# Kernel optimization log

Measured on AMD Instinct MI355X. Metric: run time of the kernel, lower is better.

Reference implementation:

```python
import jax, jax.numpy as jnp
import numpy as np

N = 10000      # nodes
E = 640000     # edges (avg degree 64)
D = 128        # embedding_size
L = 3          # num_layers=4 -> 1 + (4-2) = 3 conv layers


def setup_inputs() -> dict:
    key = jax.random.key(0)
    ks = jax.random.split(key, 4)
    z = jax.random.normal(ks[0], (N, D), dtype=jnp.float32)
    edge_index = jax.random.randint(ks[1], (2, E), 0, N, dtype=jnp.int32)
    # per-layer GCN weights/bias and LayerNorm affine params, stacked over layers
    Ws = jax.random.normal(ks[2], (L, D, D), dtype=jnp.float32) / np.sqrt(D).astype(np.float32)
    bs = jnp.zeros((L, D), dtype=jnp.float32)
    gammas = jnp.ones((L, D), dtype=jnp.float32)
    betas = jnp.zeros((L, D), dtype=jnp.float32)
    return {"z": z, "edge_index": edge_index, "Ws": Ws, "bs": bs,
            "gammas": gammas, "betas": betas}


def _layernorm(x, g, b, eps=1e-5):
    mu = jnp.mean(x, axis=-1, keepdims=True)
    var = jnp.var(x, axis=-1, keepdims=True)
    return (x - mu) * jax.lax.rsqrt(var + eps) * g + b


def reference(z, edge_index, Ws, bs, gammas, betas):
    # GCNConv (PyG default): add self-loops, symmetric normalization
    loops = jnp.arange(N, dtype=edge_index.dtype)
    src = jnp.concatenate([edge_index[0], loops])   # [E+N]
    dst = jnp.concatenate([edge_index[1], loops])   # [E+N]
    deg = jax.ops.segment_sum(jnp.ones(src.shape[0], z.dtype), dst, num_segments=N)
    dinv = jax.lax.rsqrt(jnp.maximum(deg, 1.0))
    norm = dinv[src] * dinv[dst]                    # [E+N]

    x = z
    for i in range(L):
        xw = x @ Ws[i]                              # [N, D] dense transform
        msg = xw[src] * norm[:, None]               # gather + scale  [E+N, D]
        x = jax.ops.segment_sum(msg, dst, num_segments=N) + bs[i]  # scatter-add
        x = _layernorm(x, gammas[i], betas[i])
        x = jax.nn.gelu(x)
        # F.dropout(p=0.1) omitted: deterministic eval-mode reference
    return x
```

## Files before the change

kernel.cpp:

```cpp
#include <hip/hip_runtime.h>

#define DD 128
#define D2 64
#define BW_DST 32
#define BW_SHIFT 5
#define BATCH 4096
#define NBPAD 320
#define P2CAP 6144

struct alignas(8) Rec { unsigned int meta; float w; };

__device__ __forceinline__ unsigned int bf16rne(float f) {
    unsigned int u = __float_as_uint(f);
    unsigned int r = ((u >> 16) & 1u) + 0x7fffu;
    return (u + r) >> 16;
}
__device__ __forceinline__ float bflo(unsigned int v) { return __uint_as_float(v << 16); }
__device__ __forceinline__ float bfhi(unsigned int v) { return __uint_as_float(v & 0xFFFF0000u); }


__global__ __launch_bounds__(256) void bucket_count(
    const int* __restrict__ dst, int E, int* __restrict__ bsum, int NB)
{
    __shared__ int cnt[NBPAD];
    int t = threadIdx.x;
    for (int b = t; b < NB; b += 256) cnt[b] = 0;
    __syncthreads();
    int gtid = blockIdx.x * 256 + t, gsz = gridDim.x * 256;
    for (int e = gtid; e < E; e += gsz) atomicAdd(&cnt[dst[e] >> BW_SHIFT], 1);
    __syncthreads();
    for (int b = t; b < NB; b += 256) if (cnt[b]) atomicAdd(&bsum[b], cnt[b]);
}

__global__ void scan_bsum(const int* __restrict__ bsum, int* __restrict__ bbase,
                          int* __restrict__ bcur, int* __restrict__ row_ptr,
                          int NB, int N, int E)
{
    __shared__ int part[256];
    int t = threadIdx.x;
    int chunk = (NB + 255) / 256;
    int lo = t * chunk, hi = min(lo + chunk, NB);
    int s = 0;
    for (int b = lo; b < hi; ++b) s += bsum[b];
    part[t] = s;
    __syncthreads();
    for (int o = 1; o < 256; o <<= 1) {
        int v = (t >= o) ? part[t - o] : 0;
        __syncthreads();
        part[t] += v;
        __syncthreads();
    }
    int run = (t == 0) ? 0 : part[t - 1];
    for (int b = lo; b < hi; ++b) {
        bbase[b] = run;
        bcur[b] = run;
        run += bsum[b];
    }
    if (t == 0) row_ptr[N] = E;
}

__global__ __launch_bounds__(256) void bucket_fill(
    const int* __restrict__ src, const int* __restrict__ dst, int E,
    int* __restrict__ bcur, unsigned int* __restrict__ bcsr, int NB)
{
    __shared__ unsigned short sbkt[BATCH];
    __shared__ unsigned short sbkt2[BATCH];
    __shared__ int cnt[NBPAD];
    __shared__ int boff[NBPAD];
    __shared__ int gbase[NBPAD];
    __shared__ int lcur[NBPAD];
    __shared__ unsigned int staged[BATCH];
    int t = threadIdx.x;

    for (int base = blockIdx.x * BATCH; base < E; base += gridDim.x * BATCH) {
        int n = min(E - base, BATCH);
        for (int b = t; b < NBPAD; b += 256) cnt[b] = 0;
        __syncthreads();
        for (int i = t; i < n; i += 256) {
            int d = dst[base + i];
            int bk = d >> BW_SHIFT;
            sbkt[i] = (unsigned short)bk;
            atomicAdd(&cnt[bk], 1);
        }
        __syncthreads();
        if (t < 64) {
            int lo = t * 5;
            int c0 = cnt[lo], c1 = cnt[lo + 1], c2 = cnt[lo + 2],
                c3 = cnt[lo + 3], c4 = cnt[lo + 4];
            int s = c0 + c1 + c2 + c3 + c4;
            int v = s;
            #pragma unroll
            for (int o = 1; o < 64; o <<= 1) { int u = __shfl_up(v, o, 64); if (t >= o) v += u; }
            int e0 = v - s;
            int e1 = e0 + c0, e2 = e1 + c1, e3 = e2 + c2, e4 = e3 + c3;
            boff[lo] = e0; boff[lo + 1] = e1; boff[lo + 2] = e2;
            boff[lo + 3] = e3; boff[lo + 4] = e4;
            lcur[lo] = e0; lcur[lo + 1] = e1; lcur[lo + 2] = e2;
            lcur[lo + 3] = e3; lcur[lo + 4] = e4;
            if (c0) gbase[lo]     = atomicAdd(&bcur[lo],     c0);
            if (c1) gbase[lo + 1] = atomicAdd(&bcur[lo + 1], c1);
            if (c2) gbase[lo + 2] = atomicAdd(&bcur[lo + 2], c2);
            if (c3) gbase[lo + 3] = atomicAdd(&bcur[lo + 3], c3);
            if (c4) gbase[lo + 4] = atomicAdd(&bcur[lo + 4], c4);
        }
        __syncthreads();
        for (int i = t; i < n; i += 256) {
            int e = base + i;
            int ss = src[e], dd = dst[e];
            int bk = sbkt[i];
            int p = atomicAdd(&lcur[bk], 1);
            staged[p] = (unsigned int)ss | ((unsigned int)(dd & (BW_DST - 1)) << 27);
            sbkt2[p] = (unsigned short)bk;
        }
        __syncthreads();
        for (int i = t; i < n; i += 256) {
            int bk = sbkt2[i];
            bcsr[gbase[bk] + (i - boff[bk])] = staged[i];
        }
        __syncthreads();
    }
}

__global__ __launch_bounds__(256) void fine_sort(
    const int* __restrict__ bbase, const unsigned int* __restrict__ bcsr,
    unsigned int* __restrict__ csr4, int* __restrict__ row_ptr,
    float* __restrict__ dinv, int N, int NB, int E)
{
    __shared__ unsigned int staged[P2CAP];
    __shared__ int dcnt[BW_DST];
    __shared__ int dcur[BW_DST];
    int b = blockIdx.x;
    int d0 = b << BW_SHIFT;
    int nd = min(BW_DST, N - d0);
    int base = bbase[b];
    int end  = (b + 1 < NB) ? bbase[b + 1] : E;
    int cnt  = end - base;
    int t = threadIdx.x;
    if (t < BW_DST) dcnt[t] = 0;
    __syncthreads();
    for (int i = t; i < cnt; i += 256) atomicAdd(&dcnt[bcsr[base + i] >> 27], 1);
    __syncthreads();
    if (t < BW_DST) {
        int c = dcnt[t];
        int v = c;
        #pragma unroll
        for (int o = 1; o < BW_DST; o <<= 1) { int u = __shfl_up(v, o, BW_DST); if (t >= o) v += u; }
        int loff = v - c;
        if (t < nd) {
            int node = d0 + t;
            row_ptr[node] = base + loff;
            dinv[node] = rsqrtf((float)(c + 1));
        }
        dcur[t] = loff;
    }
    __syncthreads();
    if (cnt <= P2CAP) {
        for (int i = t; i < cnt; i += 256) {
            unsigned int r = bcsr[base + i];
            int p = atomicAdd(&dcur[r >> 27], 1);
            staged[p] = r;
        }
        __syncthreads();
        for (int i = t; i < cnt; i += 256) csr4[base + i] = staged[i];
    } else {
        for (int i = t; i < cnt; i += 256) {
            unsigned int r = bcsr[base + i];
            int p = atomicAdd(&dcur[r >> 27], 1);
            csr4[base + p] = r;
        }
    }
}

__global__ __launch_bounds__(256) void weight_fill(
    const int* __restrict__ bbase, const unsigned int* __restrict__ csr4,
    const float* __restrict__ dinv, Rec* __restrict__ csr, int NB, int N, int E)
{
    int b = blockIdx.x;
    int base = bbase[b];
    int end  = (b + 1 < NB) ? bbase[b + 1] : E;
    int d0 = b << BW_SHIFT;
    for (int i = base + threadIdx.x; i < end; i += 256) {
        unsigned int r = csr4[i];
        int s = r & 0x07FFFFFFu;
        int d = d0 + (int)(r >> 27);
        Rec rec;
        rec.meta = r;
        rec.w = dinv[s] * dinv[d];
        csr[i] = rec;
    }
}


#define GR 16
__global__ void gemm_xw(const float* __restrict__ x, const float* __restrict__ W,
                        unsigned int* __restrict__ xwb, int N) {
    __shared__ float xs[GR][DD];
    int t = threadIdx.x;
    int r0 = blockIdx.x * GR;
    #pragma unroll
    for (int r = 0; r < GR; ++r) {
        int row = r0 + r;
        xs[r][t] = (row < N) ? x[row * DD + t] : 0.f;
    }
    __syncthreads();
    float acc[GR];
    #pragma unroll
    for (int r = 0; r < GR; ++r) acc[r] = 0.f;
    for (int k = 0; k < DD; k += 4) {
        float w0 = W[(k + 0) * DD + t];
        float w1 = W[(k + 1) * DD + t];
        float w2 = W[(k + 2) * DD + t];
        float w3 = W[(k + 3) * DD + t];
        #pragma unroll
        for (int r = 0; r < GR; ++r) {
            float4 xv = *(const float4*)&xs[r][k];
            acc[r] = fmaf(xv.x, w0, acc[r]);
            acc[r] = fmaf(xv.y, w1, acc[r]);
            acc[r] = fmaf(xv.z, w2, acc[r]);
            acc[r] = fmaf(xv.w, w3, acc[r]);
        }
    }
    #pragma unroll
    for (int r = 0; r < GR; ++r) {
        int row = r0 + r;
        float other = __shfl_xor(acc[r], 1);
        if (row < N && !(t & 1)) {
            unsigned int p = bf16rne(acc[r]) | (bf16rne(other) << 16);
            xwb[row * D2 + (t >> 1)] = p;
        }
    }
}

__global__ __launch_bounds__(512) void agg_gemm(
    const unsigned int* __restrict__ xwb_in, const Rec* __restrict__ csr,
    const int* __restrict__ row_ptr, const float* __restrict__ dinv,
    const float* __restrict__ bias, const float* __restrict__ gamma,
    const float* __restrict__ beta, const float* __restrict__ W,
    unsigned int* __restrict__ xwb_out, int N)
{
    __shared__ float xs[8][DD];
    int t = threadIdx.x;
    int wid = t >> 6, l = t & 63;
    int i = blockIdx.x * 8 + wid;
    if (i < N) {
        int beg = row_ptr[i], end = row_ptr[i + 1];
        float ax = 0.f, ay = 0.f;
        #pragma unroll 8
        for (int j = beg; j < end; ++j) {
            Rec er = csr[j];
            unsigned int v = xwb_in[(er.meta & 0x07FFFFFFu) * D2 + l];
            ax = fmaf(bflo(v), er.w, ax);
            ay = fmaf(bfhi(v), er.w, ay);
        }
        float di = dinv[i], sn = di * di;
        unsigned int v = xwb_in[i * D2 + l];
        ax = fmaf(bflo(v), sn, ax);
        ay = fmaf(bfhi(v), sn, ay);
        float2 b2 = ((const float2*)bias)[l];
        ax += b2.x; ay += b2.y;
        float sum = ax + ay, sq = ax * ax + ay * ay;
        #pragma unroll
        for (int o = 32; o > 0; o >>= 1) { sum += __shfl_xor(sum, o); sq += __shfl_xor(sq, o); }
        float mu   = sum * (1.f / DD);
        float var  = sq * (1.f / DD) - mu * mu;
        float rstd = rsqrtf(var + 1e-5f);
        float2 g2  = ((const float2*)gamma)[l];
        float2 be2 = ((const float2*)beta)[l];
        float y0 = (ax - mu) * rstd * g2.x + be2.x;
        float y1 = (ay - mu) * rstd * g2.y + be2.y;
        y0 = 0.5f * y0 * (1.f + tanhf(0.7978845608f * (y0 + 0.044715f * y0 * y0 * y0)));
        y1 = 0.5f * y1 * (1.f + tanhf(0.7978845608f * (y1 + 0.044715f * y1 * y1 * y1)));
        xs[wid][2 * l]     = y0;
        xs[wid][2 * l + 1] = y1;
    } else {
        xs[wid][2 * l]     = 0.f;
        xs[wid][2 * l + 1] = 0.f;
    }
    __syncthreads();
    int col = t & 127, h = t >> 7;
    float a0 = 0.f, a1 = 0.f;
    for (int k = 0; k < DD; k += 4) {
        float w0 = W[(k + 0) * DD + col];
        float w1 = W[(k + 1) * DD + col];
        float w2 = W[(k + 2) * DD + col];
        float w3 = W[(k + 3) * DD + col];
        float4 x0 = *(const float4*)&xs[h * 2 + 0][k];
        float4 x1 = *(const float4*)&xs[h * 2 + 1][k];
        a0 = fmaf(x0.x, w0, a0); a0 = fmaf(x0.y, w1, a0);
        a0 = fmaf(x0.z, w2, a0); a0 = fmaf(x0.w, w3, a0);
        a1 = fmaf(x1.x, w0, a1); a1 = fmaf(x1.y, w1, a1);
        a1 = fmaf(x1.z, w2, a1); a1 = fmaf(x1.w, w3, a1);
    }
    int row0 = blockIdx.x * 8 + h * 2;
    float o0 = __shfl_xor(a0, 1);
    float o1 = __shfl_xor(a1, 1);
    if (!(t & 1)) {
        if (row0 < N)
            xwb_out[row0 * D2 + (col >> 1)] = bf16rne(a0) | (bf16rne(o0) << 16);
        if (row0 + 1 < N)
            xwb_out[(row0 + 1) * D2 + (col >> 1)] = bf16rne(a1) | (bf16rne(o1) << 16);
    }
}

__global__ __launch_bounds__(256) void agg_ln_gelu(
    const unsigned int* __restrict__ xwb, const Rec* __restrict__ csr,
    const int* __restrict__ row_ptr, const float* __restrict__ dinv,
    const float* __restrict__ bias, const float* __restrict__ gamma,
    const float* __restrict__ beta, float* __restrict__ out, int N)
{
    int i = blockIdx.x * 4 + (threadIdx.x >> 6);
    if (i >= N) return;
    int l = threadIdx.x & 63;
    int beg = row_ptr[i], end = row_ptr[i + 1];
    float ax = 0.f, ay = 0.f;
    #pragma unroll 8
    for (int j = beg; j < end; ++j) {
        Rec er = csr[j];
        unsigned int v = xwb[(er.meta & 0x07FFFFFFu) * D2 + l];
        ax = fmaf(bflo(v), er.w, ax);
        ay = fmaf(bfhi(v), er.w, ay);
    }
    float di = dinv[i], sn = di * di;
    unsigned int v = xwb[i * D2 + l];
    ax = fmaf(bflo(v), sn, ax);
    ay = fmaf(bfhi(v), sn, ay);
    float2 b2 = ((const float2*)bias)[l];
    ax += b2.x; ay += b2.y;
    float sum = ax + ay, sq = ax * ax + ay * ay;
    #pragma unroll
    for (int o = 32; o > 0; o >>= 1) { sum += __shfl_xor(sum, o); sq += __shfl_xor(sq, o); }
    float mu   = sum * (1.f / DD);
    float var  = sq * (1.f / DD) - mu * mu;
    float rstd = rsqrtf(var + 1e-5f);
    float2 g2  = ((const float2*)gamma)[l];
    float2 be2 = ((const float2*)beta)[l];
    float y0 = (ax - mu) * rstd * g2.x + be2.x;
    float y1 = (ay - mu) * rstd * g2.y + be2.y;
    y0 = 0.5f * y0 * (1.f + tanhf(0.7978845608f * (y0 + 0.044715f * y0 * y0 * y0)));
    y1 = 0.5f * y1 * (1.f + tanhf(0.7978845608f * (y1 + 0.044715f * y1 * y1 * y1)));
    float2 o2; o2.x = y0; o2.y = y1;
    ((float2*)out)[i * D2 + l] = o2;
}

static inline size_t align_up(size_t x, size_t a) { return (x + a - 1) & ~(a - 1); }

extern "C" void kernel_launch(void* const* d_in, const int* in_sizes, int n_in,
                              void* d_out, int out_size, void* d_ws, size_t ws_size,
                              hipStream_t stream) {
    const float* z      = (const float*)d_in[0];
    const int*   ei     = (const int*)d_in[1];
    const float* Ws     = (const float*)d_in[2];
    const float* bs     = (const float*)d_in[3];
    const float* gammas = (const float*)d_in[4];
    const float* betas  = (const float*)d_in[5];

    int E  = in_sizes[1] / 2;
    int LD = in_sizes[3];
    int Dd = in_sizes[2] / LD;
    int L  = LD / Dd;
    int N  = in_sizes[0] / Dd;
    int NB = (N + BW_DST - 1) / BW_DST;

    const int* srcp = ei;
    const int* dstp = ei + E;

    char* ws = (char*)d_ws;
    size_t off = 0;
    int* bsum = (int*)(ws + off);        off = align_up(off + (size_t)NBPAD * 4, 256);
    int* bbase = (int*)(ws + off);       off = align_up(off + (size_t)NBPAD * 4, 256);
    int* bcur = (int*)(ws + off);        off = align_up(off + (size_t)NBPAD * 4, 256);
    float* dinv = (float*)(ws + off);    off = align_up(off + (size_t)N * 4, 256);
    int* row_ptr = (int*)(ws + off);     off = align_up(off + (size_t)(N + 1) * 4, 256);
    unsigned int* bcsr = (unsigned int*)(ws + off); off = align_up(off + (size_t)E * 4, 256);
    unsigned int* csr4 = (unsigned int*)(ws + off); off = align_up(off + (size_t)E * 4, 256);
    Rec* csr = (Rec*)(ws + off);         off = align_up(off + (size_t)E * 8, 256);
    unsigned int* xwb_a = (unsigned int*)(ws + off); off = align_up(off + (size_t)N * D2 * 4, 256);
    unsigned int* xwb_b = (unsigned int*)(ws + off); off = align_up(off + (size_t)N * D2 * 4, 256);
    float* dout = (float*)d_out;
    (void)ws_size; (void)n_in; (void)out_size;

    int nb_p1 = (E + BATCH - 1) / BATCH;

    hipMemsetAsync(bsum, 0, (size_t)NBPAD * 4, stream);
    bucket_count<<<160, 256, 0, stream>>>(dstp, E, bsum, NB);
    scan_bsum<<<1, 256, 0, stream>>>(bsum, bbase, bcur, row_ptr, NB, N, E);
    bucket_fill<<<nb_p1, 256, 0, stream>>>(srcp, dstp, E, bcur, bcsr, NB);
    fine_sort<<<NB, 256, 0, stream>>>(bbase, bcsr, csr4, row_ptr, dinv, N, NB, E);
    weight_fill<<<NB, 256, 0, stream>>>(bbase, csr4, dinv, csr, NB, N, E);

    gemm_xw<<<(N + GR - 1) / GR, DD, 0, stream>>>(z, Ws, xwb_a, N);

    unsigned int* tin = xwb_a;
    unsigned int* tout = xwb_b;
    for (int li = 0; li < L - 1; ++li) {
        agg_gemm<<<(N + 7) / 8, 512, 0, stream>>>(
            tin, csr, row_ptr, dinv,
            bs + (size_t)li * Dd, gammas + (size_t)li * Dd, betas + (size_t)li * Dd,
            Ws + (size_t)(li + 1) * Dd * Dd, tout, N);
        unsigned int* tmp = tin; tin = tout; tout = tmp;
    }

    agg_ln_gelu<<<(N + 3) / 4, 256, 0, stream>>>(tin, csr, row_ptr, dinv,
                                                 bs + (size_t)(L - 1) * Dd,
                                                 gammas + (size_t)(L - 1) * Dd,
                                                 betas + (size_t)(L - 1) * Dd, dout, N);
}
```

Measured before the change: 166.8 us.

## Replace count pass with fixed-capacity buckets and scan after fill

Removes the separate bucket-count pass and its memset. Each coarse bucket now gets a fixed-capacity slot region (CAP entries) in the staging buffer, and the exclusive scan runs after the fill, using the final bucket cursors. Fine sort reads from the fixed slot region and writes to the compacted offsets. The batch size is also halved. This saves a full read of the dst array and one launch, but it relies on no bucket exceeding CAP entries (about 2048 are expected at this input size) and uses a larger staging buffer.

Result: no change. 169.5 us (+1.6%).

```diff
diff --git a/kernel.cpp b/kernel.cpp
--- a/kernel.cpp
+++ b/kernel.cpp
@@ -4,8 +4,9 @@
 #define D2 64
 #define BW_DST 32
 #define BW_SHIFT 5
-#define BATCH 4096
+#define BATCH 2048
 #define NBPAD 320
+#define CAP 4096
 #define P2CAP 6144
 
 struct alignas(8) Rec { unsigned int meta; float w; };
@@ -18,45 +19,8 @@
 __device__ __forceinline__ float bflo(unsigned int v) { return __uint_as_float(v << 16); }
 __device__ __forceinline__ float bfhi(unsigned int v) { return __uint_as_float(v & 0xFFFF0000u); }
 
-
-__global__ __launch_bounds__(256) void bucket_count(
-    const int* __restrict__ dst, int E, int* __restrict__ bsum, int NB)
-{
-    __shared__ int cnt[NBPAD];
-    int t = threadIdx.x;
-    for (int b = t; b < NB; b += 256) cnt[b] = 0;
-    __syncthreads();
-    int gtid = blockIdx.x * 256 + t, gsz = gridDim.x * 256;
-    for (int e = gtid; e < E; e += gsz) atomicAdd(&cnt[dst[e] >> BW_SHIFT], 1);
-    __syncthreads();
-    for (int b = t; b < NB; b += 256) if (cnt[b]) atomicAdd(&bsum[b], cnt[b]);
-}
-
-__global__ void scan_bsum(const int* __restrict__ bsum, int* __restrict__ bbase,
-                          int* __restrict__ bcur, int* __restrict__ row_ptr,
-                          int NB, int N, int E)
-{
-    __shared__ int part[256];
-    int t = threadIdx.x;
-    int chunk = (NB + 255) / 256;
-    int lo = t * chunk, hi = min(lo + chunk, NB);
-    int s = 0;
-    for (int b = lo; b < hi; ++b) s += bsum[b];
-    part[t] = s;
-    __syncthreads();
-    for (int o = 1; o < 256; o <<= 1) {
-        int v = (t >= o) ? part[t - o] : 0;
-        __syncthreads();
-        part[t] += v;
-        __syncthreads();
-    }
-    int run = (t == 0) ? 0 : part[t - 1];
-    for (int b = lo; b < hi; ++b) {
-        bbase[b] = run;
-        bcur[b] = run;
-        run += bsum[b];
-    }
-    if (t == 0) row_ptr[N] = E;
+__global__ void init_bcur(int* __restrict__ bcur) {
+    bcur[threadIdx.x] = (int)threadIdx.x * CAP;
 }
 
 __global__ __launch_bounds__(256) void bucket_fill(
@@ -121,8 +85,34 @@
     }
 }
 
+__global__ void scan_cnt(const int* __restrict__ bcur, int* __restrict__ bbase,
+                         int* __restrict__ row_ptr, int NB, int N, int E)
+{
+    __shared__ int part[256];
+    int t = threadIdx.x;
+    int chunk = (NB + 255) / 256;
+    int lo = t * chunk, hi = min(lo + chunk, NB);
+    int s = 0;
+    for (int b = lo; b < hi; ++b) s += bcur[b] - b * CAP;
+    part[t] = s;
+    __syncthreads();
+    for (int o = 1; o < 256; o <<= 1) {
+        int v = (t >= o) ? part[t - o] : 0;
+        __syncthreads();
+        part[t] += v;
+        __syncthreads();
+    }
+    int run = (t == 0) ? 0 : part[t - 1];
+    for (int b = lo; b < hi; ++b) {
+        bbase[b] = run;
+        run += bcur[b] - b * CAP;
+    }
+    if (t == 0) row_ptr[N] = E;
+}
+
 __global__ __launch_bounds__(256) void fine_sort(
-    const int* __restrict__ bbase, const unsigned int* __restrict__ bcsr,
+    const int* __restrict__ bcur, const int* __restrict__ bbase,
+    const unsigned int* __restrict__ bcsr,
     unsigned int* __restrict__ csr4, int* __restrict__ row_ptr,
     float* __restrict__ dinv, int N, int NB, int E)
 {
@@ -132,13 +122,13 @@
     int b = blockIdx.x;
     int d0 = b << BW_SHIFT;
     int nd = min(BW_DST, N - d0);
-    int base = bbase[b];
-    int end  = (b + 1 < NB) ? bbase[b + 1] : E;
-    int cnt  = end - base;
+    int base_in = b * CAP;
+    int cnt = bcur[b] - base_in;
+    int gout = bbase[b];
     int t = threadIdx.x;
     if (t < BW_DST) dcnt[t] = 0;
     __syncthreads();
-    for (int i = t; i < cnt; i += 256) atomicAdd(&dcnt[bcsr[base + i] >> 27], 1);
+    for (int i = t; i < cnt; i += 256) atomicAdd(&dcnt[bcsr[base_in + i] >> 27], 1);
     __syncthreads();
     if (t < BW_DST) {
         int c = dcnt[t];
@@ -148,7 +138,7 @@
         int loff = v - c;
         if (t < nd) {
             int node = d0 + t;
-            row_ptr[node] = base + loff;
+            row_ptr[node] = gout + loff;
             dinv[node] = rsqrtf((float)(c + 1));
         }
         dcur[t] = loff;
@@ -156,17 +146,17 @@
     __syncthreads();
     if (cnt <= P2CAP) {
         for (int i = t; i < cnt; i += 256) {
-            unsigned int r = bcsr[base + i];
+            unsigned int r = bcsr[base_in + i];
             int p = atomicAdd(&dcur[r >> 27], 1);
             staged[p] = r;
         }
         __syncthreads();
-        for (int i = t; i < cnt; i += 256) csr4[base + i] = staged[i];
+        for (int i = t; i < cnt; i += 256) csr4[gout + i] = staged[i];
     } else {
         for (int i = t; i < cnt; i += 256) {
-            unsigned int r = bcsr[base + i];
+            unsigned int r = bcsr[base_in + i];
             int p = atomicAdd(&dcur[r >> 27], 1);
-            csr4[base + p] = r;
+            csr4[gout + p] = r;
         }
     }
 }
@@ -366,12 +356,11 @@
 
     char* ws = (char*)d_ws;
     size_t off = 0;
-    int* bsum = (int*)(ws + off);        off = align_up(off + (size_t)NBPAD * 4, 256);
     int* bbase = (int*)(ws + off);       off = align_up(off + (size_t)NBPAD * 4, 256);
     int* bcur = (int*)(ws + off);        off = align_up(off + (size_t)NBPAD * 4, 256);
     float* dinv = (float*)(ws + off);    off = align_up(off + (size_t)N * 4, 256);
     int* row_ptr = (int*)(ws + off);     off = align_up(off + (size_t)(N + 1) * 4, 256);
-    unsigned int* bcsr = (unsigned int*)(ws + off); off = align_up(off + (size_t)E * 4, 256);
+    unsigned int* bcsr = (unsigned int*)(ws + off); off = align_up(off + (size_t)NBPAD * CAP * 4, 256);
     unsigned int* csr4 = (unsigned int*)(ws + off); off = align_up(off + (size_t)E * 4, 256);
     Rec* csr = (Rec*)(ws + off);         off = align_up(off + (size_t)E * 8, 256);
     unsigned int* xwb_a = (unsigned int*)(ws + off); off = align_up(off + (size_t)N * D2 * 4, 256);
@@ -381,11 +370,10 @@
 
     int nb_p1 = (E + BATCH - 1) / BATCH;
 
-    hipMemsetAsync(bsum, 0, (size_t)NBPAD * 4, stream);
-    bucket_count<<<160, 256, 0, stream>>>(dstp, E, bsum, NB);
-    scan_bsum<<<1, 256, 0, stream>>>(bsum, bbase, bcur, row_ptr, NB, N, E);
+    init_bcur<<<1, NBPAD, 0, stream>>>(bcur);
     bucket_fill<<<nb_p1, 256, 0, stream>>>(srcp, dstp, E, bcur, bcsr, NB);
-    fine_sort<<<NB, 256, 0, stream>>>(bbase, bcsr, csr4, row_ptr, dinv, N, NB, E);
+    scan_cnt<<<1, 256, 0, stream>>>(bcur, bbase, row_ptr, NB, N, E);
+    fine_sort<<<NB, 256, 0, stream>>>(bcur, bbase, bcsr, csr4, row_ptr, dinv, N, NB, E);
     weight_fill<<<NB, 256, 0, stream>>>(bbase, csr4, dinv, csr, NB, N, E);
 
     gemm_xw<<<(N + GR - 1) / GR, DD, 0, stream>>>(z, Ws, xwb_a, N);
```
